# Kernel optimization log

Hardware: AMD Instinct MI355X
Metric: run time of the kernel (lower is better)

The kernel has to match this reference:

```python
import jax, jax.numpy as jnp
import numpy as np

N_NODES = 100000
N_EDGES = 640000
D_IN = 128
D_HID = 128
D_OUT = 128
EPS = 1e-12  # F.normalize clamp_min eps


def _sage_conv(x, src, dst, Wl, bl, Wr):
    # mean aggregation of source features onto destination nodes
    msgs = x[src]                                              # [E, C] gather
    agg = jax.ops.segment_sum(msgs, dst, num_segments=N_NODES)  # [N, C] scatter-add
    cnt = jax.ops.segment_sum(jnp.ones((src.shape[0],), x.dtype), dst,
                              num_segments=N_NODES)
    agg = agg / jnp.maximum(cnt, 1.0)[:, None]
    out = agg @ Wl.T + bl + x @ Wr.T                           # lin_l(aggr) + lin_r(root)
    # L2 row-normalize (normalize=True)
    norm = jnp.sqrt(jnp.sum(out * out, axis=-1, keepdims=True))
    return out / jnp.maximum(norm, EPS)


def setup_inputs() -> dict:
    key = jax.random.key(0)
    ks = jax.random.split(key, 8)
    x = jax.random.normal(ks[0], (N_NODES, D_IN), dtype=jnp.float32)
    edge_index = jax.random.randint(ks[1], (2, N_EDGES), 0, N_NODES, dtype=jnp.int64)
    s1 = 1.0 / np.sqrt(D_IN)
    s2 = 1.0 / np.sqrt(D_HID)
    Wl1 = jax.random.uniform(ks[2], (D_HID, D_IN), jnp.float32, -s1, s1)
    bl1 = jax.random.uniform(ks[3], (D_HID,), jnp.float32, -s1, s1)
    Wr1 = jax.random.uniform(ks[4], (D_HID, D_IN), jnp.float32, -s1, s1)
    Wl2 = jax.random.uniform(ks[5], (D_OUT, D_HID), jnp.float32, -s2, s2)
    bl2 = jax.random.uniform(ks[6], (D_OUT,), jnp.float32, -s2, s2)
    Wr2 = jax.random.uniform(ks[7], (D_OUT, D_HID), jnp.float32, -s2, s2)
    return {"x": x, "edge_index": edge_index, "Wl1": Wl1, "bl1": bl1,
            "Wr1": Wr1, "Wl2": Wl2, "bl2": bl2, "Wr2": Wr2}


def reference(x, edge_index, Wl1, bl1, Wr1, Wl2, bl2, Wr2):
    src, dst = edge_index[0], edge_index[1]
    h = _sage_conv(x, src, dst, Wl1, bl1, Wr1)
    h = jax.nn.relu(h)  # dropout is identity in eval mode
    h = _sage_conv(h, src, dst, Wl2, bl2, Wr2)
    return h
```

## Files before the change

kernel.cpp:

```cpp
#include <hip/hip_runtime.h>
#include <hip/hip_bf16.h>
#include <stdint.h>

#define N_NODES 100000
#define N_EDGES 640000
#define MPAD    100096
#define CONV_T  (N_NODES * 64)

typedef short  bf8_t  __attribute__((ext_vector_type(8)));
typedef float  f32x4  __attribute__((ext_vector_type(4)));

__device__ __forceinline__ unsigned f2bf(float f) {
  unsigned u = __builtin_bit_cast(unsigned, f);
  return ((u + 0x7fffu + ((u >> 16) & 1u)) >> 16) & 0xffffu;
}
__device__ __forceinline__ float bf2f(unsigned bits) {
  return __builtin_bit_cast(float, bits << 16);
}

__global__ void k_count(const int* __restrict__ dst, int* __restrict__ cnt) {
  int e = blockIdx.x * blockDim.x + threadIdx.x;
  if (e < N_EDGES) atomicAdd(&cnt[dst[e]], 1);
}

__global__ void k_bsum(const int* __restrict__ cnt, int* __restrict__ bsum) {
  __shared__ int s[256];
  int base = blockIdx.x * 1024;
  int t = threadIdx.x;
  int v = 0;
  for (int j = 0; j < 4; ++j) {
    int i = base + j * 256 + t;
    if (i < N_NODES) v += cnt[i];
  }
  s[t] = v; __syncthreads();
  for (int o = 128; o > 0; o >>= 1) { if (t < o) s[t] += s[t + o]; __syncthreads(); }
  if (t == 0) bsum[blockIdx.x] = s[0];
}

__global__ void k_scanb(int* __restrict__ bsum, int nb) {
  __shared__ int s[128];
  int t = threadIdx.x;
  int v = (t < nb) ? bsum[t] : 0;
  s[t] = v; __syncthreads();
  for (int o = 1; o < 128; o <<= 1) {
    int add = (t >= o) ? s[t - o] : 0;
    __syncthreads();
    s[t] += add;
    __syncthreads();
  }
  if (t < nb) bsum[t] = s[t] - v;
}

__global__ void k_scanchunk(const int* __restrict__ cnt, const int* __restrict__ bsum,
                            int* __restrict__ rowptr, float* __restrict__ inv) {
  __shared__ int s[1024];
  int t = threadIdx.x;
  int i = blockIdx.x * 1024 + t;
  int v = (i < N_NODES) ? cnt[i] : 0;
  s[t] = v; __syncthreads();
  for (int o = 1; o < 1024; o <<= 1) {
    int add = (t >= o) ? s[t - o] : 0;
    __syncthreads();
    s[t] += add;
    __syncthreads();
  }
  int incl = s[t];
  int bofs = bsum[blockIdx.x];
  if (i < N_NODES) {
    rowptr[i] = bofs + incl - v;
    inv[i] = 1.0f / fmaxf((float)v, 1.0f);
  }
  if (i == N_NODES - 1) rowptr[N_NODES] = bofs + incl;
}

__global__ void k_scatter(const int* __restrict__ src, const int* __restrict__ dst,
                          const int* __restrict__ rowptr, int* __restrict__ cursor,
                          int* __restrict__ esrc) {
  int e = blockIdx.x * blockDim.x + threadIdx.x;
  if (e < N_EDGES) {
    int d = dst[e];
    int p = atomicAdd(&cursor[d], 1);
    esrc[rowptr[d] + p] = src[e];
  }
}

__global__ void k_prep(const float* __restrict__ x, unsigned* __restrict__ A1,
                       const float* __restrict__ Wl1, const float* __restrict__ Wr1,
                       unsigned short* __restrict__ Bf1,
                       const float* __restrict__ Wl2, const float* __restrict__ Wr2,
                       unsigned short* __restrict__ Bf2) {
  int i = blockIdx.x * blockDim.x + threadIdx.x;
  if (i < CONV_T) {
    int w = i >> 6, lane = i & 63;
    float2 v = ((const float2*)x)[i];
    A1[(size_t)w * 128 + 64 + lane] = f2bf(v.x) | (f2bf(v.y) << 16);
    return;
  }
  int gid = i - CONV_T;
  if (gid >= 8192) return;
  int tid = gid & 4095;
  const float* Wl = (gid < 4096) ? Wl1 : Wl2;
  const float* Wr = (gid < 4096) ? Wr1 : Wr2;
  unsigned short* Bf = (gid < 4096) ? Bf1 : Bf2;
  int lane = tid & 63;
  int t  = (tid >> 6) & 7;
  int kc = tid >> 9;
  int c = lane & 15, q = lane >> 4;
  int col = t * 16 + c;
  for (int j = 0; j < 8; ++j) {
    int k = kc * 32 + q * 8 + j;
    float v = (k < 128) ? Wl[col * 128 + k] : Wr[col * 128 + (k - 128)];
    Bf[(size_t)tid * 8 + j] = (unsigned short)f2bf(v);
  }
}

__global__ __launch_bounds__(256) void k_agg(const unsigned* __restrict__ A,
    const int* __restrict__ rowptr, const int* __restrict__ esrc,
    const float* __restrict__ inv) {
  int w = (blockIdx.x * blockDim.x + threadIdx.x) >> 6;
  int lane = threadIdx.x & 63;
  if (w >= N_NODES) return;
  int b = rowptr[w], e = rowptr[w + 1];
  int deg = e - b;
  int myi = (lane < deg) ? esrc[b + lane] : 0;
  float ax = 0.f, ay = 0.f;
  int n = (deg < 64) ? deg : 64;
  for (int j0 = 0; j0 < n; j0 += 8) {
    unsigned u[8];
#pragma unroll
    for (int j = 0; j < 8; ++j) {
      int s = __shfl(myi, j0 + j);
      u[j] = A[(size_t)s * 128 + 64 + lane];
    }
#pragma unroll
    for (int j = 0; j < 8; ++j) {
      if (j0 + j < n) { ax += bf2f(u[j] & 0xffffu); ay += bf2f(u[j] >> 16); }
    }
  }
  for (int j = b + 64; j < e; ++j) {
    int s = esrc[j];
    unsigned u = A[(size_t)s * 128 + 64 + lane];
    ax += bf2f(u & 0xffffu); ay += bf2f(u >> 16);
  }
  float iv = inv[w];
  ((unsigned*)A)[(size_t)w * 128 + lane] = f2bf(ax * iv) | (f2bf(ay * iv) << 16);
}

template<int LAYER>
__global__ __launch_bounds__(128) void k_gemm(const unsigned short* __restrict__ A,
    const unsigned short* __restrict__ Bf, const float* __restrict__ bias,
    void* __restrict__ outp) {
  int wid = threadIdx.x >> 6;
  int lane = threadIdx.x & 63;
  int c = lane & 15, q = lane >> 4;
  int m0 = blockIdx.x * 64 + wid * 32;
  bf8_t a0[8], a1[8];
#pragma unroll
  for (int kc = 0; kc < 8; ++kc) {
    a0[kc] = *(const bf8_t*)(A + (size_t)(m0 + c) * 256 + kc * 32 + q * 8);
    a1[kc] = *(const bf8_t*)(A + (size_t)(m0 + 16 + c) * 256 + kc * 32 + q * 8);
  }
  f32x4 acc[2][8];
#pragma unroll
  for (int h = 0; h < 2; ++h)
#pragma unroll
    for (int t = 0; t < 8; ++t) acc[h][t] = (f32x4){0.f, 0.f, 0.f, 0.f};
  const bf8_t* Bv = (const bf8_t*)Bf;
#pragma unroll
  for (int kc = 0; kc < 8; ++kc) {
#pragma unroll
    for (int t = 0; t < 8; ++t) {
      bf8_t b = Bv[(kc * 8 + t) * 64 + lane];
      acc[0][t] = __builtin_amdgcn_mfma_f32_16x16x32_bf16(a0[kc], b, acc[0][t], 0, 0, 0);
      acc[1][t] = __builtin_amdgcn_mfma_f32_16x16x32_bf16(a1[kc], b, acc[1][t], 0, 0, 0);
    }
  }
  float bcol[8];
#pragma unroll
  for (int t = 0; t < 8; ++t) bcol[t] = bias[t * 16 + c];
#pragma unroll
  for (int h = 0; h < 2; ++h) {
#pragma unroll
    for (int r = 0; r < 4; ++r) {
      float ss = 0.f;
#pragma unroll
      for (int t = 0; t < 8; ++t) {
        float v = acc[h][t][r] + bcol[t];
        acc[h][t][r] = v;
        ss += v * v;
      }
#pragma unroll
      for (int m = 1; m < 16; m <<= 1) ss += __shfl_xor(ss, m, 64);
      float invn = 1.0f / fmaxf(sqrtf(ss), 1e-12f);
      int row = m0 + h * 16 + q * 4 + r;
      if (row < N_NODES) {
        if (LAYER == 1) {
          unsigned short* o = (unsigned short*)outp;
#pragma unroll
          for (int t = 0; t < 8; ++t) {
            float v = fmaxf(acc[h][t][r] * invn, 0.f);
            o[(size_t)row * 256 + 128 + t * 16 + c] = (unsigned short)f2bf(v);
          }
        } else {
          float* o = (float*)outp;
#pragma unroll
          for (int t = 0; t < 8; ++t)
            o[(size_t)row * 128 + t * 16 + c] = acc[h][t][r] * invn;
        }
      }
    }
  }
}

extern "C" void kernel_launch(void* const* d_in, const int* in_sizes, int n_in,
                              void* d_out, int out_size, void* d_ws, size_t ws_size,
                              hipStream_t stream) {
  const float* x   = (const float*)d_in[0];
  const int*   ei  = (const int*)d_in[1];
  const int*   src = ei;
  const int*   dst = ei + N_EDGES;
  const float* Wl1 = (const float*)d_in[2];
  const float* bl1 = (const float*)d_in[3];
  const float* Wr1 = (const float*)d_in[4];
  const float* Wl2 = (const float*)d_in[5];
  const float* bl2 = (const float*)d_in[6];
  const float* Wr2 = (const float*)d_in[7];

  char* ws = (char*)d_ws;
  size_t off = 0;
  auto alloc = [&](size_t bytes) -> void* {
    void* p = ws + off;
    off += (bytes + 255) & ~(size_t)255;
    return p;
  };
  unsigned short* A1  = (unsigned short*)alloc((size_t)MPAD * 256 * 2);
  unsigned short* A2  = (unsigned short*)alloc((size_t)MPAD * 256 * 2);
  unsigned short* Bf1 = (unsigned short*)alloc(65536);
  unsigned short* Bf2 = (unsigned short*)alloc(65536);
  int*   esrc   = (int*)alloc((size_t)N_EDGES * 4);
  int*   rowptr = (int*)alloc((size_t)(N_NODES + 1) * 4);
  int*   cnt    = (int*)alloc((size_t)N_NODES * 4);
  int*   cursor = (int*)alloc((size_t)N_NODES * 4);
  float* inv    = (float*)alloc((size_t)N_NODES * 4);
  int*   bsum   = (int*)alloc(1024);

  const size_t cntR = ((size_t)N_NODES * 4 + 255) & ~(size_t)255;
  hipMemsetAsync(cnt, 0, 2 * cntR, stream);

  const int NB = (N_NODES + 1023) / 1024;
  k_count    <<<(N_EDGES + 255) / 256, 256, 0, stream>>>(dst, cnt);
  k_bsum     <<<NB, 256, 0, stream>>>(cnt, bsum);
  k_scanb    <<<1, 128, 0, stream>>>(bsum, NB);
  k_scanchunk<<<NB, 1024, 0, stream>>>(cnt, bsum, rowptr, inv);
  k_scatter  <<<(N_EDGES + 255) / 256, 256, 0, stream>>>(src, dst, rowptr, cursor, esrc);
  k_prep     <<<(CONV_T + 8192 + 255) / 256, 256, 0, stream>>>(
                 x, (unsigned*)A1, Wl1, Wr1, Bf1, Wl2, Wr2, Bf2);

  k_agg    <<<(N_NODES * 64 + 255) / 256, 256, 0, stream>>>((unsigned*)A1, rowptr, esrc, inv);
  k_gemm<1><<<MPAD / 64, 128, 0, stream>>>(A1, Bf1, bl1, A2);
  k_agg    <<<(N_NODES * 64 + 255) / 256, 256, 0, stream>>>((unsigned*)A2, rowptr, esrc, inv);
  k_gemm<2><<<MPAD / 64, 128, 0, stream>>>(A2, Bf2, bl2, d_out);
}
```

Before: 312.1 us.

## Fuse count with prep, stage GEMM weights in LDS, pack layer-1 stores

Merges the edge-degree count and the input/weight conversion into one launch, removing a kernel launch and letting the two independent jobs overlap. The GEMM now uses 256-thread blocks of 128 rows and loads the 64KB bf16 weight tile into shared memory once per block, instead of every wave reading it from global memory. Layer-1 outputs are packed into 32-bit bf16 pairs via a lane shuffle, halving the number of store instructions. The large LDS allocation may limit how many blocks fit on each CU.

```diff
diff --git a/kernel.cpp b/kernel.cpp
--- a/kernel.cpp
+++ b/kernel.cpp
@@ -6,6 +6,7 @@
 #define N_EDGES 640000
 #define MPAD    100096
 #define CONV_T  (N_NODES * 64)
+#define EDGE_BLOCKS ((N_EDGES + 255) / 256)
 
 typedef short  bf8_t  __attribute__((ext_vector_type(8)));
 typedef float  f32x4  __attribute__((ext_vector_type(4)));
@@ -18,78 +19,18 @@
   return __builtin_bit_cast(float, bits << 16);
 }
 
-__global__ void k_count(const int* __restrict__ dst, int* __restrict__ cnt) {
-  int e = blockIdx.x * blockDim.x + threadIdx.x;
-  if (e < N_EDGES) atomicAdd(&cnt[dst[e]], 1);
-}
-
-__global__ void k_bsum(const int* __restrict__ cnt, int* __restrict__ bsum) {
-  __shared__ int s[256];
-  int base = blockIdx.x * 1024;
-  int t = threadIdx.x;
-  int v = 0;
-  for (int j = 0; j < 4; ++j) {
-    int i = base + j * 256 + t;
-    if (i < N_NODES) v += cnt[i];
-  }
-  s[t] = v; __syncthreads();
-  for (int o = 128; o > 0; o >>= 1) { if (t < o) s[t] += s[t + o]; __syncthreads(); }
-  if (t == 0) bsum[blockIdx.x] = s[0];
-}
-
-__global__ void k_scanb(int* __restrict__ bsum, int nb) {
-  __shared__ int s[128];
-  int t = threadIdx.x;
-  int v = (t < nb) ? bsum[t] : 0;
-  s[t] = v; __syncthreads();
-  for (int o = 1; o < 128; o <<= 1) {
-    int add = (t >= o) ? s[t - o] : 0;
-    __syncthreads();
-    s[t] += add;
-    __syncthreads();
-  }
-  if (t < nb) bsum[t] = s[t] - v;
-}
-
-__global__ void k_scanchunk(const int* __restrict__ cnt, const int* __restrict__ bsum,
-                            int* __restrict__ rowptr, float* __restrict__ inv) {
-  __shared__ int s[1024];
-  int t = threadIdx.x;
-  int i = blockIdx.x * 1024 + t;
-  int v = (i < N_NODES) ? cnt[i] : 0;
-  s[t] = v; __syncthreads();
-  for (int o = 1; o < 1024; o <<= 1) {
-    int add = (t >= o) ? s[t - o] : 0;
-    __syncthreads();
-    s[t] += add;
-    __syncthreads();
-  }
-  int incl = s[t];
-  int bofs = bsum[blockIdx.x];
-  if (i < N_NODES) {
-    rowptr[i] = bofs + incl - v;
-    inv[i] = 1.0f / fmaxf((float)v, 1.0f);
-  }
-  if (i == N_NODES - 1) rowptr[N_NODES] = bofs + incl;
-}
-
-__global__ void k_scatter(const int* __restrict__ src, const int* __restrict__ dst,
-                          const int* __restrict__ rowptr, int* __restrict__ cursor,
-                          int* __restrict__ esrc) {
-  int e = blockIdx.x * blockDim.x + threadIdx.x;
-  if (e < N_EDGES) {
-    int d = dst[e];
-    int p = atomicAdd(&cursor[d], 1);
-    esrc[rowptr[d] + p] = src[e];
-  }
-}
-
-__global__ void k_prep(const float* __restrict__ x, unsigned* __restrict__ A1,
-                       const float* __restrict__ Wl1, const float* __restrict__ Wr1,
-                       unsigned short* __restrict__ Bf1,
-                       const float* __restrict__ Wl2, const float* __restrict__ Wr2,
-                       unsigned short* __restrict__ Bf2) {
-  int i = blockIdx.x * blockDim.x + threadIdx.x;
+__global__ void k_count_prep(const int* __restrict__ dst, int* __restrict__ cnt,
+                             const float* __restrict__ x, unsigned* __restrict__ A1,
+                             const float* __restrict__ Wl1, const float* __restrict__ Wr1,
+                             unsigned short* __restrict__ Bf1,
+                             const float* __restrict__ Wl2, const float* __restrict__ Wr2,
+                             unsigned short* __restrict__ Bf2) {
+  if (blockIdx.x < EDGE_BLOCKS) {
+    int e = blockIdx.x * 256 + threadIdx.x;
+    if (e < N_EDGES) atomicAdd(&cnt[dst[e]], 1);
+    return;
+  }
+  int i = (blockIdx.x - EDGE_BLOCKS) * 256 + threadIdx.x;
   if (i < CONV_T) {
     int w = i >> 6, lane = i & 63;
     float2 v = ((const float2*)x)[i];
@@ -114,6 +55,67 @@
   }
 }
 
+__global__ void k_bsum(const int* __restrict__ cnt, int* __restrict__ bsum) {
+  __shared__ int s[256];
+  int base = blockIdx.x * 1024;
+  int t = threadIdx.x;
+  int v = 0;
+  for (int j = 0; j < 4; ++j) {
+    int i = base + j * 256 + t;
+    if (i < N_NODES) v += cnt[i];
+  }
+  s[t] = v; __syncthreads();
+  for (int o = 128; o > 0; o >>= 1) { if (t < o) s[t] += s[t + o]; __syncthreads(); }
+  if (t == 0) bsum[blockIdx.x] = s[0];
+}
+
+__global__ void k_scanb(int* __restrict__ bsum, int nb) {
+  __shared__ int s[128];
+  int t = threadIdx.x;
+  int v = (t < nb) ? bsum[t] : 0;
+  s[t] = v; __syncthreads();
+  for (int o = 1; o < 128; o <<= 1) {
+    int add = (t >= o) ? s[t - o] : 0;
+    __syncthreads();
+    s[t] += add;
+    __syncthreads();
+  }
+  if (t < nb) bsum[t] = s[t] - v;
+}
+
+__global__ void k_scanchunk(const int* __restrict__ cnt, const int* __restrict__ bsum,
+                            int* __restrict__ rowptr, float* __restrict__ inv) {
+  __shared__ int s[1024];
+  int t = threadIdx.x;
+  int i = blockIdx.x * 1024 + t;
+  int v = (i < N_NODES) ? cnt[i] : 0;
+  s[t] = v; __syncthreads();
+  for (int o = 1; o < 1024; o <<= 1) {
+    int add = (t >= o) ? s[t - o] : 0;
+    __syncthreads();
+    s[t] += add;
+    __syncthreads();
+  }
+  int incl = s[t];
+  int bofs = bsum[blockIdx.x];
+  if (i < N_NODES) {
+    rowptr[i] = bofs + incl - v;
+    inv[i] = 1.0f / fmaxf((float)v, 1.0f);
+  }
+  if (i == N_NODES - 1) rowptr[N_NODES] = bofs + incl;
+}
+
+__global__ void k_scatter(const int* __restrict__ src, const int* __restrict__ dst,
+                          const int* __restrict__ rowptr, int* __restrict__ cursor,
+                          int* __restrict__ esrc) {
+  int e = blockIdx.x * blockDim.x + threadIdx.x;
+  if (e < N_EDGES) {
+    int d = dst[e];
+    int p = atomicAdd(&cursor[d], 1);
+    esrc[rowptr[d] + p] = src[e];
+  }
+}
+
 __global__ __launch_bounds__(256) void k_agg(const unsigned* __restrict__ A,
     const int* __restrict__ rowptr, const int* __restrict__ esrc,
     const float* __restrict__ inv) {
@@ -147,25 +149,32 @@
 }
 
 template<int LAYER>
-__global__ __launch_bounds__(128) void k_gemm(const unsigned short* __restrict__ A,
+__global__ __launch_bounds__(256) void k_gemm(const unsigned short* __restrict__ A,
     const unsigned short* __restrict__ Bf, const float* __restrict__ bias,
     void* __restrict__ outp) {
+  __shared__ unsigned short Bs[32768];
   int wid = threadIdx.x >> 6;
   int lane = threadIdx.x & 63;
   int c = lane & 15, q = lane >> 4;
-  int m0 = blockIdx.x * 64 + wid * 32;
+  int m0 = blockIdx.x * 128 + wid * 32;
+
   bf8_t a0[8], a1[8];
 #pragma unroll
   for (int kc = 0; kc < 8; ++kc) {
     a0[kc] = *(const bf8_t*)(A + (size_t)(m0 + c) * 256 + kc * 32 + q * 8);
     a1[kc] = *(const bf8_t*)(A + (size_t)(m0 + 16 + c) * 256 + kc * 32 + q * 8);
   }
+#pragma unroll
+  for (int i = 0; i < 16; ++i)
+    ((bf8_t*)Bs)[i * 256 + threadIdx.x] = ((const bf8_t*)Bf)[i * 256 + threadIdx.x];
+  __syncthreads();
+
   f32x4 acc[2][8];
 #pragma unroll
   for (int h = 0; h < 2; ++h)
 #pragma unroll
     for (int t = 0; t < 8; ++t) acc[h][t] = (f32x4){0.f, 0.f, 0.f, 0.f};
-  const bf8_t* Bv = (const bf8_t*)Bf;
+  const bf8_t* Bv = (const bf8_t*)Bs;
 #pragma unroll
   for (int kc = 0; kc < 8; ++kc) {
 #pragma unroll
@@ -193,16 +202,18 @@
       for (int m = 1; m < 16; m <<= 1) ss += __shfl_xor(ss, m, 64);
       float invn = 1.0f / fmaxf(sqrtf(ss), 1e-12f);
       int row = m0 + h * 16 + q * 4 + r;
-      if (row < N_NODES) {
-        if (LAYER == 1) {
-          unsigned short* o = (unsigned short*)outp;
-#pragma unroll
-          for (int t = 0; t < 8; ++t) {
-            float v = fmaxf(acc[h][t][r] * invn, 0.f);
-            o[(size_t)row * 256 + 128 + t * 16 + c] = (unsigned short)f2bf(v);
-          }
-        } else {
-          float* o = (float*)outp;
+      if (LAYER == 1) {
+        unsigned* o32 = (unsigned*)outp;
+#pragma unroll
+        for (int t = 0; t < 8; ++t) {
+          float v = fmaxf(acc[h][t][r] * invn, 0.f);
+          float vp = __shfl_xor(v, 1, 64);
+          if (row < N_NODES && !(c & 1))
+            o32[(size_t)row * 128 + 64 + t * 8 + (c >> 1)] = f2bf(v) | (f2bf(vp) << 16);
+        }
+      } else {
+        float* o = (float*)outp;
+        if (row < N_NODES) {
 #pragma unroll
           for (int t = 0; t < 8; ++t)
             o[(size_t)row * 128 + t * 16 + c] = acc[h][t][r] * invn;
@@ -248,16 +259,16 @@
   hipMemsetAsync(cnt, 0, 2 * cntR, stream);
 
   const int NB = (N_NODES + 1023) / 1024;
-  k_count    <<<(N_EDGES + 255) / 256, 256, 0, stream>>>(dst, cnt);
+  const int PREP_BLOCKS = (CONV_T + 8192 + 255) / 256;
+  k_count_prep<<<EDGE_BLOCKS + PREP_BLOCKS, 256, 0, stream>>>(
+                 dst, cnt, x, (unsigned*)A1, Wl1, Wr1, Bf1, Wl2, Wr2, Bf2);
   k_bsum     <<<NB, 256, 0, stream>>>(cnt, bsum);
   k_scanb    <<<1, 128, 0, stream>>>(bsum, NB);
   k_scanchunk<<<NB, 1024, 0, stream>>>(cnt, bsum, rowptr, inv);
   k_scatter  <<<(N_EDGES + 255) / 256, 256, 0, stream>>>(src, dst, rowptr, cursor, esrc);
-  k_prep     <<<(CONV_T + 8192 + 255) / 256, 256, 0, stream>>>(
-                 x, (unsigned*)A1, Wl1, Wr1, Bf1, Wl2, Wr2, Bf2);
 
   k_agg    <<<(N_NODES * 64 + 255) / 256, 256, 0, stream>>>((unsigned*)A1, rowptr, esrc, inv);
-  k_gemm<1><<<MPAD / 64, 128, 0, stream>>>(A1, Bf1, bl1, A2);
+  k_gemm<1><<<MPAD / 128, 256, 0, stream>>>(A1, Bf1, bl1, A2);
   k_agg    <<<(N_NODES * 64 + 255) / 256, 256, 0, stream>>>((unsigned*)A2, rowptr, esrc, inv);
-  k_gemm<2><<<MPAD / 64, 128, 0, stream>>>(A2, Bf2, bl2, d_out);
-}
+  k_gemm<2><<<MPAD / 128, 256, 0, stream>>>(A2, Bf2, bl2, d_out);
+}
```

After: 299.5 us. -4.0%, faster.
